# Optimization experiments

Measured on AMD Instinct MI355X. Metric: run time of the kernel, lower is better.

## Reference

```python
import jax, jax.numpy as jnp
import numpy as np

ROPE_BASE = 100.0  # CroCo/InfiniteVGGT-style 2D RoPE base

def _rope_1d(sub, pos, base=ROPE_BASE):
    # sub: (B,H,N,half), pos: (B,N) float
    half = sub.shape[-1]
    quarter = half // 2
    inv_freq = 1.0 / (base ** (jnp.arange(quarter, dtype=jnp.float32) / quarter))
    ang = pos[:, None, :, None] * inv_freq  # (B,1,N,quarter)
    cos, sin = jnp.cos(ang), jnp.sin(ang)
    x1, x2 = sub[..., :quarter], sub[..., quarter:]
    return jnp.concatenate([x1 * cos - x2 * sin, x1 * sin + x2 * cos], axis=-1)

def rope_2d(t, positions):
    # t: (B,H,N,Dh); positions: (B,N,2) int (y,x)
    Dh = t.shape[-1]
    half = Dh // 2
    pos_f = positions.astype(t.dtype)
    y = _rope_1d(t[..., :half], pos_f[..., 0])
    x = _rope_1d(t[..., half:], pos_f[..., 1])
    return jnp.concatenate([y, x], axis=-1)

def setup_inputs() -> dict:
    key = jax.random.key(0)
    k1, k2, k3, k4 = jax.random.split(key, 4)
    B, N, C, H = 2, 2048, 1024, 16
    x = jax.random.normal(k1, (B, N, C), dtype=jnp.float32)
    positions = jax.random.randint(k2, (B, N, 2), 0, 64, dtype=jnp.int32)
    qkv_w = jax.random.normal(k3, (3 * C, C), dtype=jnp.float32) * (C ** -0.5)
    proj_w = jax.random.normal(k4, (C, C), dtype=jnp.float32) * (C ** -0.5)
    proj_b = jnp.zeros((C,), dtype=jnp.float32)
    return {"x": x, "positions": positions, "qkv_w": qkv_w, "proj_w": proj_w, "proj_b": proj_b}

def reference(x, positions, qkv_w, proj_w, proj_b):
    B, N, C = x.shape
    H = 16
    Dh = C // H
    scale = Dh ** -0.5
    qkv = (x @ qkv_w.T).reshape(B, N, 3, H, Dh).transpose(2, 0, 3, 1, 4)  # (3,B,H,N,Dh)
    q, k, v = qkv[0], qkv[1], qkv[2]
    q = rope_2d(q, positions)
    k = rope_2d(k, positions)
    attn = jnp.einsum('bhnd,bhmd->bhnm', q, k) * scale  # (B,H,N,N)
    attn = jax.nn.softmax(attn, axis=-1)
    out = jnp.einsum('bhnm,bhmd->bhnd', attn, v)  # (B,H,N,Dh)
    out = out.transpose(0, 2, 1, 3).reshape(B, N, C)
    return out @ proj_w.T + proj_b
```

## Files before the change

kernel.cpp:

```cpp
#include <hip/hip_runtime.h>

typedef unsigned short u16;
typedef unsigned int   u32;
typedef __attribute__((ext_vector_type(8))) __bf16 bf16x8;
typedef __attribute__((ext_vector_type(4))) float  f32x4;

constexpr int BB = 2, SEQ = 2048, CH = 1024, NH = 16, DH = 64;

__device__ inline u16 f2bf(float f) {
    u32 u = __builtin_bit_cast(u32, f);
    u += 0x7FFF + ((u >> 16) & 1);
    return (u16)(u >> 16);
}
__device__ inline float bf2f(u16 b) { return __builtin_bit_cast(float, (u32)b << 16); }
__device__ inline u32 pkbf(float a, float b) {
    return (u32)f2bf(a) | ((u32)f2bf(b) << 16);
}
__device__ inline float fexp2(float x) {
#if __has_builtin(__builtin_amdgcn_exp2f)
    return __builtin_amdgcn_exp2f(x);
#else
    return exp2f(x);
#endif
}

__device__ inline void gld_lds16(const void* g, void* l) {
    __builtin_amdgcn_global_load_lds((const __attribute__((address_space(1))) void*)g,
                                     (__attribute__((address_space(3))) void*)l, 16, 0, 0);
}
__device__ inline f32x4 mfma16(bf16x8 a, bf16x8 b, f32x4 c) {
    return __builtin_amdgcn_mfma_f32_16x16x32_bf16(a, b, c, 0, 0, 0);
}
__device__ inline bf16x8 ld_frag(const u16* p) {
    return __builtin_bit_cast(bf16x8, *(const uint4*)p);
}

__global__ __launch_bounds__(256) void convert_kernel(const float* __restrict__ x,
                                                      const float* __restrict__ wq,
                                                      const float* __restrict__ wp,
                                                      u16* __restrict__ xb,
                                                      u16* __restrict__ wqb,
                                                      u16* __restrict__ wpb) {
    const int q = blockIdx.x * 256 + threadIdx.x;
    const float* src; u16* dst; int idx;
    if (q < 1048576)            { src = x;  dst = xb;  idx = q; }
    else if (q < 1048576+786432){ src = wq; dst = wqb; idx = q - 1048576; }
    else                        { src = wp; dst = wpb; idx = q - 1048576 - 786432; }
    float4 v = *(const float4*)(src + (size_t)idx * 4);
    ushort4 o; o.x = f2bf(v.x); o.y = f2bf(v.y); o.z = f2bf(v.z); o.w = f2bf(v.w);
    *(ushort4*)(dst + (size_t)idx * 4) = o;
}

__global__ __launch_bounds__(256) void gemm_bf16(const u16* __restrict__ A,
                                                 const u16* __restrict__ Bw,
                                                 const float* __restrict__ bias,
                                                 void* __restrict__ Cout,
                                                 int M, int N, int K, int out_fp32) {
    __shared__ u16 As[128 * 32];
    __shared__ u16 Bs[128 * 32];
    const int t = threadIdx.x, lane = t & 63, w = t >> 6;
    const int l15 = lane & 15, quad = lane >> 4;
    const int wm = w >> 1, wn = w & 1;
    const int m0 = blockIdx.y * 128, n0 = blockIdx.x * 128;

    const int row0 = t >> 2, v0 = t & 3;
    const int gi0 = (v0 - (row0 >> 1)) & 3;
    const int row1 = row0 + 64;
    const int gi1 = (v0 - (row1 >> 1)) & 3;

    f32x4 acc[4][4] = {};
    for (int k0 = 0; k0 < K; k0 += 32) {
        __syncthreads();
        gld_lds16(A  + (size_t)(m0 + row0) * K + k0 + gi0 * 8, As + t * 8);
        gld_lds16(A  + (size_t)(m0 + row1) * K + k0 + gi1 * 8, As + 2048 + t * 8);
        gld_lds16(Bw + (size_t)(n0 + row0) * K + k0 + gi0 * 8, Bs + t * 8);
        gld_lds16(Bw + (size_t)(n0 + row1) * K + k0 + gi1 * 8, Bs + 2048 + t * 8);
        __syncthreads();
        bf16x8 af[4], bfv[4];
#pragma unroll
        for (int mi = 0; mi < 4; ++mi) {
            const int r = wm * 64 + mi * 16 + l15;
            af[mi] = ld_frag(As + (r * 4 + ((quad + (r >> 1)) & 3)) * 8);
        }
#pragma unroll
        for (int nj = 0; nj < 4; ++nj) {
            const int r = wn * 64 + nj * 16 + l15;
            bfv[nj] = ld_frag(Bs + (r * 4 + ((quad + (r >> 1)) & 3)) * 8);
        }
#pragma unroll
        for (int mi = 0; mi < 4; ++mi)
#pragma unroll
            for (int nj = 0; nj < 4; ++nj)
                acc[mi][nj] = mfma16(af[mi], bfv[nj], acc[mi][nj]);
    }
    if (out_fp32) {
        float* C = (float*)Cout;
#pragma unroll
        for (int mi = 0; mi < 4; ++mi)
#pragma unroll
            for (int nj = 0; nj < 4; ++nj) {
                const int n = n0 + wn * 64 + nj * 16 + l15;
                const float bv = bias ? bias[n] : 0.0f;
#pragma unroll
                for (int r = 0; r < 4; ++r) {
                    const int m = m0 + wm * 64 + mi * 16 + quad * 4 + r;
                    C[(size_t)m * N + n] = acc[mi][nj][r] + bv;
                }
            }
    } else {
        u16* C = (u16*)Cout;
#pragma unroll
        for (int mi = 0; mi < 4; ++mi)
#pragma unroll
            for (int nj = 0; nj < 4; ++nj) {
                const int n = n0 + wn * 64 + nj * 16 + l15;
#pragma unroll
                for (int r = 0; r < 4; ++r) {
                    const int m = m0 + wm * 64 + mi * 16 + quad * 4 + r;
                    C[(size_t)m * N + n] = f2bf(acc[mi][nj][r]);
                }
            }
    }
}

__global__ __launch_bounds__(256) void rope_pack(const u16* __restrict__ qkv,
                                                 const int* __restrict__ pos,
                                                 u16* __restrict__ Qb,
                                                 u16* __restrict__ Kb,
                                                 u16* __restrict__ Vt) {
    __shared__ u16 vlds[64 * 68];
    const int t = threadIdx.x;
    const int r = t >> 2, s = t & 3;
    const int bh = blockIdx.y, b = bh >> 4;
    const int n0 = blockIdx.x * 64;
    const int bn = b * SEQ + n0 + r;
    const float py = (float)pos[bn * 2], px = (float)pos[bn * 2 + 1];

    float cy[4], sy[4], cx[4], sx[4];
#pragma unroll
    for (int j = 0; j < 4; ++j) {
        const int i = s * 4 + j;
        const float f = exp2f(-(float)i * 0.41524101186092f);
        sincosf(py * f, &sy[j], &cy[j]);
        sincosf(px * f, &sx[j], &cx[j]);
    }
    const size_t rowb = (size_t)bn * (3 * CH) + (bh & 15) * 64;

#pragma unroll
    for (int wk = 0; wk < 2; ++wk) {
        const u16* src = qkv + rowb + wk * CH;
        u16* dst = (wk ? Kb : Qb) + ((size_t)bh * SEQ + n0 + r) * 64;
        ushort4 a0 = *(const ushort4*)(src + s * 4);
        ushort4 a1 = *(const ushort4*)(src + s * 4 + 16);
        ushort4 a2 = *(const ushort4*)(src + s * 4 + 32);
        ushort4 a3 = *(const ushort4*)(src + s * 4 + 48);
        const float scale = wk ? 1.0f : 0.18033688011112042f;
        ushort4 o0, o1, o2, o3;
#pragma unroll
        for (int j = 0; j < 4; ++j) {
            const float x1 = bf2f(((const u16*)&a0)[j]), x2 = bf2f(((const u16*)&a1)[j]);
            ((u16*)&o0)[j] = f2bf((x1 * cy[j] - x2 * sy[j]) * scale);
            ((u16*)&o1)[j] = f2bf((x1 * sy[j] + x2 * cy[j]) * scale);
            const float y1 = bf2f(((const u16*)&a2)[j]), y2 = bf2f(((const u16*)&a3)[j]);
            ((u16*)&o2)[j] = f2bf((y1 * cx[j] - y2 * sx[j]) * scale);
            ((u16*)&o3)[j] = f2bf((y1 * sx[j] + y2 * cx[j]) * scale);
        }
        *(ushort4*)(dst + s * 4)      = o0;
        *(ushort4*)(dst + s * 4 + 16) = o1;
        *(ushort4*)(dst + s * 4 + 32) = o2;
        *(ushort4*)(dst + s * 4 + 48) = o3;
    }
    {
        const u16* src = qkv + rowb + 2 * CH;
#pragma unroll
        for (int jj = 0; jj < 4; ++jj) {
            ushort4 v = *(const ushort4*)(src + s * 16 + jj * 4);
#pragma unroll
            for (int j = 0; j < 4; ++j)
                vlds[(s * 16 + jj * 4 + j) * 68 + r] = ((const u16*)&v)[j];
        }
        __syncthreads();
        const int d = r;
        u16* gdst = Vt + ((size_t)bh * 64 + d) * SEQ + n0 + s * 16;
#pragma unroll
        for (int jj = 0; jj < 4; ++jj)
            *(ushort4*)(gdst + jj * 4) = *(const ushort4*)(vlds + d * 68 + s * 16 + jj * 4);
    }
}

__global__ __launch_bounds__(256, 4) void attn_mfma(const u16* __restrict__ Qb,
                                                    const u16* __restrict__ Kb,
                                                    const u16* __restrict__ Vt,
                                                    u16* __restrict__ Opart,
                                                    float* __restrict__ lpart) {
    __shared__ u16 Ks[64 * 64];
    __shared__ u16 Vs[64 * 64];
    __shared__ u16 Ps[128 * 72];
    const int t = threadIdx.x, lane = t & 63, w = t >> 6;
    const int l15 = lane & 15, quad = lane >> 4;
    const int bh = blockIdx.y;
    const int q0 = blockIdx.x * 128;
    const int z  = blockIdx.z;

    const int rowA = t >> 3, vA = t & 7;
    const int giA = (vA - rowA) & 7;
    const int rowB = rowA + 32;
    const int giB = (vA - rowB) & 7;

    const size_t kbase = (size_t)bh * SEQ * 64;
    const size_t vbase = (size_t)bh * 64 * SEQ;

    bf16x8 aq[2][2];
#pragma unroll
    for (int mi = 0; mi < 2; ++mi)
#pragma unroll
        for (int ks = 0; ks < 2; ++ks)
            aq[mi][ks] = ld_frag(Qb + ((size_t)bh * SEQ + q0 + w * 32 + mi * 16 + l15) * 64
                                 + ks * 32 + quad * 8);

    f32x4 oacc[2][4] = {};
    float lsum[2] = {0.0f, 0.0f};

    for (int kt = 0; kt < 16; ++kt) {
        const int k0 = z * 1024 + kt * 64;
        __syncthreads();
        gld_lds16(Kb + kbase + (size_t)(k0 + rowA) * 64 + giA * 8, Ks + t * 8);
        gld_lds16(Kb + kbase + (size_t)(k0 + rowB) * 64 + giB * 8, Ks + 2048 + t * 8);
        gld_lds16(Vt + vbase + (size_t)rowA * SEQ + k0 + giA * 8, Vs + t * 8);
        gld_lds16(Vt + vbase + (size_t)rowB * SEQ + k0 + giB * 8, Vs + 2048 + t * 8);
        __syncthreads();

        f32x4 sacc[2][4] = {};
#pragma unroll
        for (int ks = 0; ks < 2; ++ks)
#pragma unroll
            for (int nk = 0; nk < 4; ++nk) {
                const int rK = nk * 16 + l15;
                const bf16x8 kf = ld_frag(Ks + (rK * 8 + (((ks * 4 + quad) + rK) & 7)) * 8);
                sacc[0][nk] = mfma16(kf, aq[0][ks], sacc[0][nk]);
                sacc[1][nk] = mfma16(kf, aq[1][ks], sacc[1][nk]);
            }

#pragma unroll
        for (int mi = 0; mi < 2; ++mi) {
            const int prow = (w * 32 + mi * 16 + l15) * 72;
#pragma unroll
            for (int nk = 0; nk < 4; ++nk) {
                const float p0 = fexp2(sacc[mi][nk][0]);
                const float p1 = fexp2(sacc[mi][nk][1]);
                const float p2 = fexp2(sacc[mi][nk][2]);
                const float p3 = fexp2(sacc[mi][nk][3]);
                lsum[mi] += (p0 + p1) + (p2 + p3);
                uint2 pk; pk.x = pkbf(p0, p1); pk.y = pkbf(p2, p3);
                *(uint2*)&Ps[prow + nk * 16 + quad * 4] = pk;
            }
        }

#pragma unroll
        for (int ks = 0; ks < 2; ++ks) {
            const bf16x8 ap0 = ld_frag(Ps + (w * 32 + l15) * 72 + ks * 32 + quad * 8);
            const bf16x8 ap1 = ld_frag(Ps + (w * 32 + 16 + l15) * 72 + ks * 32 + quad * 8);
#pragma unroll
            for (int nj = 0; nj < 4; ++nj) {
                const int rV = nj * 16 + l15;
                const bf16x8 vf = ld_frag(Vs + (rV * 8 + (((ks * 4 + quad) + rV) & 7)) * 8);
                oacc[0][nj] = mfma16(ap0, vf, oacc[0][nj]);
                oacc[1][nj] = mfma16(ap1, vf, oacc[1][nj]);
            }
        }
    }

#pragma unroll
    for (int mi = 0; mi < 2; ++mi) {
        lsum[mi] += __shfl_xor(lsum[mi], 16);
        lsum[mi] += __shfl_xor(lsum[mi], 32);
        if (quad == 0)
            lpart[((size_t)z * 32 + bh) * SEQ + q0 + w * 32 + mi * 16 + l15] = lsum[mi];
#pragma unroll
        for (int r = 0; r < 4; ++r) {
            const int qrow = q0 + w * 32 + mi * 16 + quad * 4 + r;
            const size_t orow = (((size_t)z * 32 + bh) * SEQ + qrow) * 64;
#pragma unroll
            for (int nj = 0; nj < 4; ++nj)
                Opart[orow + nj * 16 + l15] = f2bf(oacc[mi][nj][r]);
        }
    }
}

__global__ __launch_bounds__(256) void merge_kernel(const u16* __restrict__ Opart,
                                                    const float* __restrict__ lpart,
                                                    u16* __restrict__ Ob) {
    const int gid = blockIdx.x * 256 + threadIdx.x;
    const int d4 = gid & 15, q = (gid >> 4) & 2047, bh = gid >> 15;
    const size_t i1 = ((size_t)bh * SEQ + q) * 64 + d4 * 4;
    const size_t i2 = i1 + (size_t)32 * SEQ * 64;
    const float inv = 1.0f / (lpart[(size_t)bh * SEQ + q] +
                              lpart[(size_t)(32 + bh) * SEQ + q]);
    const ushort4 a = *(const ushort4*)(Opart + i1);
    const ushort4 b = *(const ushort4*)(Opart + i2);
    ushort4 o;
    o.x = f2bf((bf2f(a.x) + bf2f(b.x)) * inv);
    o.y = f2bf((bf2f(a.y) + bf2f(b.y)) * inv);
    o.z = f2bf((bf2f(a.z) + bf2f(b.z)) * inv);
    o.w = f2bf((bf2f(a.w) + bf2f(b.w)) * inv);
    const int b_ = bh >> 4, h = bh & 15;
    *(ushort4*)(Ob + ((size_t)(b_ * SEQ + q)) * CH + h * 64 + d4 * 4) = o;
}

extern "C" void kernel_launch(void* const* d_in, const int* in_sizes, int n_in,
                              void* d_out, int out_size, void* d_ws, size_t ws_size,
                              hipStream_t stream) {
    const float* x      = (const float*)d_in[0];
    const int*   pos    = (const int*)d_in[1];
    const float* qkv_w  = (const float*)d_in[2];
    const float* proj_w = (const float*)d_in[3];
    const float* proj_b = (const float*)d_in[4];
    float* out = (float*)d_out;

    u16* ws = (u16*)d_ws;
    u16* qkv_bf  = ws;
    u16* Opart   = ws;
    u16* attn_bf = ws + 8388608;
    u16* x_bf    = ws + 12582912;
    u16* Qb      = x_bf;
    u16* wq_bf   = ws + 16777216;
    float* lpart = (float*)(ws + 16777216);
    u16* wp_bf   = ws + 19922944;
    u16* Kb      = ws + 20971520;
    u16* Vt      = ws + 25165824;

    const int M = BB * SEQ;

    convert_kernel<<<8192, 256, 0, stream>>>(x, qkv_w, proj_w, x_bf, wq_bf, wp_bf);
    gemm_bf16<<<dim3(3 * CH / 128, M / 128), 256, 0, stream>>>(
        x_bf, wq_bf, nullptr, qkv_bf, M, 3 * CH, CH, 0);
    rope_pack<<<dim3(SEQ / 64, BB * NH), 256, 0, stream>>>(qkv_bf, pos, Qb, Kb, Vt);
    attn_mfma<<<dim3(SEQ / 128, BB * NH, 2), 256, 0, stream>>>(Qb, Kb, Vt, Opart, lpart);
    merge_kernel<<<4096, 256, 0, stream>>>(Opart, lpart, attn_bf);
    gemm_bf16<<<dim3(CH / 128, M / 128), 256, 0, stream>>>(
        attn_bf, wp_bf, proj_b, out, M, CH, CH, 1);
}
```

Baseline: 215.0 us.

## Fuse RoPE and V transpose into QKV GEMM epilogue; MFMA row sums

Drops the separate rope_pack kernel. The QKV GEMM epilogue now applies RoPE and the Q scale directly to the accumulators and writes Q/K in head layout, and it transposes V through LDS before writing it out. This removes the round trip of the intermediate bf16 QKV tensor through memory and one kernel launch. In attention, the softmax row sums are now computed by an extra MFMA against a vector of ones on the bf16 P tile instead of scalar adds and shuffles, and pkbf uses the hardware packed bf16 convert when it is available. The costs are per-element sincos in the GEMM epilogue, scattered 2-byte stores for Q/K, and row sums taken from the rounded bf16 probabilities.

```diff
diff --git a/kernel.cpp b/kernel.cpp
--- a/kernel.cpp
+++ b/kernel.cpp
@@ -1,8 +1,10 @@
 #include <hip/hip_runtime.h>
+#include <cmath>
 
 typedef unsigned short u16;
 typedef unsigned int   u32;
 typedef __attribute__((ext_vector_type(8))) __bf16 bf16x8;
+typedef __attribute__((ext_vector_type(2))) __bf16 bf16x2;
 typedef __attribute__((ext_vector_type(4))) float  f32x4;
 
 constexpr int BB = 2, SEQ = 2048, CH = 1024, NH = 16, DH = 64;
@@ -14,7 +16,12 @@
 }
 __device__ inline float bf2f(u16 b) { return __builtin_bit_cast(float, (u32)b << 16); }
 __device__ inline u32 pkbf(float a, float b) {
+#if __has_builtin(__builtin_amdgcn_cvt_pk_bf16_f32)
+    bf16x2 r = __builtin_amdgcn_cvt_pk_bf16_f32(a, b);
+    return __builtin_bit_cast(u32, r);
+#else
     return (u32)f2bf(a) | ((u32)f2bf(b) << 16);
+#endif
 }
 __device__ inline float fexp2(float x) {
 #if __has_builtin(__builtin_amdgcn_exp2f)
@@ -51,11 +58,103 @@
     *(ushort4*)(dst + (size_t)idx * 4) = o;
 }
 
+__global__ __launch_bounds__(256) void gemm_qkv_rope(const u16* __restrict__ A,
+                                                     const u16* __restrict__ Bw,
+                                                     const int* __restrict__ pos,
+                                                     u16* __restrict__ Qb,
+                                                     u16* __restrict__ Kb,
+                                                     u16* __restrict__ Vt) {
+    __shared__ u16 smem[18432];
+    u16* As = smem;
+    u16* Bs = smem + 4096;
+    const int t = threadIdx.x, lane = t & 63, w = t >> 6;
+    const int l15 = lane & 15, quad = lane >> 4;
+    const int wm = w >> 1, wn = w & 1;
+    const int m0 = blockIdx.y * 128, n0 = blockIdx.x * 128;
+    const int K = CH, N = 3 * CH;
+
+    const int row0 = t >> 2, v0 = t & 3;
+    const int gi0 = (v0 - (row0 >> 1)) & 3;
+    const int row1 = row0 + 64;
+    const int gi1 = (v0 - (row1 >> 1)) & 3;
+
+    f32x4 acc[4][4] = {};
+    for (int k0 = 0; k0 < K; k0 += 32) {
+        __syncthreads();
+        gld_lds16(A  + (size_t)(m0 + row0) * K + k0 + gi0 * 8, As + t * 8);
+        gld_lds16(A  + (size_t)(m0 + row1) * K + k0 + gi1 * 8, As + 2048 + t * 8);
+        gld_lds16(Bw + (size_t)(n0 + row0) * K + k0 + gi0 * 8, Bs + t * 8);
+        gld_lds16(Bw + (size_t)(n0 + row1) * K + k0 + gi1 * 8, Bs + 2048 + t * 8);
+        __syncthreads();
+        bf16x8 af[4], bfv[4];
+#pragma unroll
+        for (int mi = 0; mi < 4; ++mi) {
+            const int r = wm * 64 + mi * 16 + l15;
+            af[mi] = ld_frag(As + (r * 4 + ((quad + (r >> 1)) & 3)) * 8);
+        }
+#pragma unroll
+        for (int nj = 0; nj < 4; ++nj) {
+            const int r = wn * 64 + nj * 16 + l15;
+            bfv[nj] = ld_frag(Bs + (r * 4 + ((quad + (r >> 1)) & 3)) * 8);
+        }
+#pragma unroll
+        for (int mi = 0; mi < 4; ++mi)
+#pragma unroll
+            for (int nj = 0; nj < 4; ++nj)
+                acc[mi][nj] = mfma16(af[mi], bfv[nj], acc[mi][nj]);
+    }
+
+    const int reg = n0 >> 10;
+    const int h   = ((n0 & 1023) >> 6) + wn;
+    if (reg < 2) {
+        const float fr = exp2f(-(float)l15 * 0.41524101186092f);
+        const float scale = reg ? 1.0f : 0.18033688011112042f;
+        u16* dst = reg ? Kb : Qb;
+#pragma unroll
+        for (int mi = 0; mi < 4; ++mi) {
+#pragma unroll
+            for (int r = 0; r < 4; ++r) {
+                const int m = m0 + wm * 64 + mi * 16 + quad * 4 + r;
+                const int bh = (m >> 11) * NH + h;
+                const int n  = m & 2047;
+                float sy, cy, sx, cx;
+                sincosf((float)pos[m * 2]     * fr, &sy, &cy);
+                sincosf((float)pos[m * 2 + 1] * fr, &sx, &cx);
+                cy *= scale; sy *= scale; cx *= scale; sx *= scale;
+                const float x1 = acc[mi][0][r], x2 = acc[mi][1][r];
+                const float y1 = acc[mi][2][r], y2 = acc[mi][3][r];
+                u16* p = dst + ((size_t)bh * SEQ + n) * 64 + l15;
+                p[0]  = f2bf(x1 * cy - x2 * sy);
+                p[16] = f2bf(x1 * sy + x2 * cy);
+                p[32] = f2bf(y1 * cx - y2 * sx);
+                p[48] = f2bf(y1 * sx + y2 * cx);
+            }
+        }
+    } else {
+        __syncthreads();
+        u16* T = smem + w * 4608;
+#pragma unroll
+        for (int mi = 0; mi < 4; ++mi)
+#pragma unroll
+            for (int nj = 0; nj < 4; ++nj)
+#pragma unroll
+                for (int r = 0; r < 4; ++r)
+                    T[(nj * 16 + l15) * 72 + mi * 16 + quad * 4 + r] =
+                        f2bf(acc[mi][nj][r]);
+        const int bh = (m0 >> 11) * NH + h;
+        const int nbase = (m0 & 2047) + wm * 64;
+        u16* gdst = Vt + ((size_t)bh * 64 + lane) * SEQ + nbase;
+#pragma unroll
+        for (int j = 0; j < 8; ++j)
+            *(uint4*)(gdst + j * 8) = *(const uint4*)(T + lane * 72 + j * 8);
+    }
+}
+
 __global__ __launch_bounds__(256) void gemm_bf16(const u16* __restrict__ A,
                                                  const u16* __restrict__ Bw,
                                                  const float* __restrict__ bias,
-                                                 void* __restrict__ Cout,
-                                                 int M, int N, int K, int out_fp32) {
+                                                 float* __restrict__ C,
+                                                 int M, int N, int K) {
     __shared__ u16 As[128 * 32];
     __shared__ u16 Bs[128 * 32];
     const int t = threadIdx.x, lane = t & 63, w = t >> 6;
@@ -93,99 +192,18 @@
             for (int nj = 0; nj < 4; ++nj)
                 acc[mi][nj] = mfma16(af[mi], bfv[nj], acc[mi][nj]);
     }
-    if (out_fp32) {
-        float* C = (float*)Cout;
-#pragma unroll
-        for (int mi = 0; mi < 4; ++mi)
-#pragma unroll
-            for (int nj = 0; nj < 4; ++nj) {
-                const int n = n0 + wn * 64 + nj * 16 + l15;
-                const float bv = bias ? bias[n] : 0.0f;
-#pragma unroll
-                for (int r = 0; r < 4; ++r) {
-                    const int m = m0 + wm * 64 + mi * 16 + quad * 4 + r;
-                    C[(size_t)m * N + n] = acc[mi][nj][r] + bv;
-                }
-            }
-    } else {
-        u16* C = (u16*)Cout;
-#pragma unroll
-        for (int mi = 0; mi < 4; ++mi)
-#pragma unroll
-            for (int nj = 0; nj < 4; ++nj) {
-                const int n = n0 + wn * 64 + nj * 16 + l15;
-#pragma unroll
-                for (int r = 0; r < 4; ++r) {
-                    const int m = m0 + wm * 64 + mi * 16 + quad * 4 + r;
-                    C[(size_t)m * N + n] = f2bf(acc[mi][nj][r]);
-                }
-            }
-    }
-}
-
-__global__ __launch_bounds__(256) void rope_pack(const u16* __restrict__ qkv,
-                                                 const int* __restrict__ pos,
-                                                 u16* __restrict__ Qb,
-                                                 u16* __restrict__ Kb,
-                                                 u16* __restrict__ Vt) {
-    __shared__ u16 vlds[64 * 68];
-    const int t = threadIdx.x;
-    const int r = t >> 2, s = t & 3;
-    const int bh = blockIdx.y, b = bh >> 4;
-    const int n0 = blockIdx.x * 64;
-    const int bn = b * SEQ + n0 + r;
-    const float py = (float)pos[bn * 2], px = (float)pos[bn * 2 + 1];
-
-    float cy[4], sy[4], cx[4], sx[4];
-#pragma unroll
-    for (int j = 0; j < 4; ++j) {
-        const int i = s * 4 + j;
-        const float f = exp2f(-(float)i * 0.41524101186092f);
-        sincosf(py * f, &sy[j], &cy[j]);
-        sincosf(px * f, &sx[j], &cx[j]);
-    }
-    const size_t rowb = (size_t)bn * (3 * CH) + (bh & 15) * 64;
-
-#pragma unroll
-    for (int wk = 0; wk < 2; ++wk) {
-        const u16* src = qkv + rowb + wk * CH;
-        u16* dst = (wk ? Kb : Qb) + ((size_t)bh * SEQ + n0 + r) * 64;
-        ushort4 a0 = *(const ushort4*)(src + s * 4);
-        ushort4 a1 = *(const ushort4*)(src + s * 4 + 16);
-        ushort4 a2 = *(const ushort4*)(src + s * 4 + 32);
-        ushort4 a3 = *(const ushort4*)(src + s * 4 + 48);
-        const float scale = wk ? 1.0f : 0.18033688011112042f;
-        ushort4 o0, o1, o2, o3;
-#pragma unroll
-        for (int j = 0; j < 4; ++j) {
-            const float x1 = bf2f(((const u16*)&a0)[j]), x2 = bf2f(((const u16*)&a1)[j]);
-            ((u16*)&o0)[j] = f2bf((x1 * cy[j] - x2 * sy[j]) * scale);
-            ((u16*)&o1)[j] = f2bf((x1 * sy[j] + x2 * cy[j]) * scale);
-            const float y1 = bf2f(((const u16*)&a2)[j]), y2 = bf2f(((const u16*)&a3)[j]);
-            ((u16*)&o2)[j] = f2bf((y1 * cx[j] - y2 * sx[j]) * scale);
-            ((u16*)&o3)[j] = f2bf((y1 * sx[j] + y2 * cx[j]) * scale);
-        }
-        *(ushort4*)(dst + s * 4)      = o0;
-        *(ushort4*)(dst + s * 4 + 16) = o1;
-        *(ushort4*)(dst + s * 4 + 32) = o2;
-        *(ushort4*)(dst + s * 4 + 48) = o3;
-    }
-    {
-        const u16* src = qkv + rowb + 2 * CH;
-#pragma unroll
-        for (int jj = 0; jj < 4; ++jj) {
-            ushort4 v = *(const ushort4*)(src + s * 16 + jj * 4);
-#pragma unroll
-            for (int j = 0; j < 4; ++j)
-                vlds[(s * 16 + jj * 4 + j) * 68 + r] = ((const u16*)&v)[j];
-        }
-        __syncthreads();
-        const int d = r;
-        u16* gdst = Vt + ((size_t)bh * 64 + d) * SEQ + n0 + s * 16;
-#pragma unroll
-        for (int jj = 0; jj < 4; ++jj)
-            *(ushort4*)(gdst + jj * 4) = *(const ushort4*)(vlds + d * 68 + s * 16 + jj * 4);
-    }
+#pragma unroll
+    for (int mi = 0; mi < 4; ++mi)
+#pragma unroll
+        for (int nj = 0; nj < 4; ++nj) {
+            const int n = n0 + wn * 64 + nj * 16 + l15;
+            const float bv = bias[n];
+#pragma unroll
+            for (int r = 0; r < 4; ++r) {
+                const int m = m0 + wm * 64 + mi * 16 + quad * 4 + r;
+                C[(size_t)m * N + n] = acc[mi][nj][r] + bv;
+            }
+        }
 }
 
 __global__ __launch_bounds__(256, 4) void attn_mfma(const u16* __restrict__ Qb,
@@ -210,6 +228,9 @@
     const size_t kbase = (size_t)bh * SEQ * 64;
     const size_t vbase = (size_t)bh * 64 * SEQ;
 
+    const uint4 ones_u = {0x3F803F80u, 0x3F803F80u, 0x3F803F80u, 0x3F803F80u};
+    const bf16x8 onesf = __builtin_bit_cast(bf16x8, ones_u);
+
     bf16x8 aq[2][2];
 #pragma unroll
     for (int mi = 0; mi < 2; ++mi)
@@ -219,7 +240,7 @@
                                  + ks * 32 + quad * 8);
 
     f32x4 oacc[2][4] = {};
-    float lsum[2] = {0.0f, 0.0f};
+    f32x4 lacc[2] = {};
 
     for (int kt = 0; kt < 16; ++kt) {
         const int k0 = z * 1024 + kt * 64;
@@ -250,7 +271,6 @@
                 const float p1 = fexp2(sacc[mi][nk][1]);
                 const float p2 = fexp2(sacc[mi][nk][2]);
                 const float p3 = fexp2(sacc[mi][nk][3]);
-                lsum[mi] += (p0 + p1) + (p2 + p3);
                 uint2 pk; pk.x = pkbf(p0, p1); pk.y = pkbf(p2, p3);
                 *(uint2*)&Ps[prow + nk * 16 + quad * 4] = pk;
             }
@@ -260,6 +280,8 @@
         for (int ks = 0; ks < 2; ++ks) {
             const bf16x8 ap0 = ld_frag(Ps + (w * 32 + l15) * 72 + ks * 32 + quad * 8);
             const bf16x8 ap1 = ld_frag(Ps + (w * 32 + 16 + l15) * 72 + ks * 32 + quad * 8);
+            lacc[0] = mfma16(ap0, onesf, lacc[0]);
+            lacc[1] = mfma16(ap1, onesf, lacc[1]);
 #pragma unroll
             for (int nj = 0; nj < 4; ++nj) {
                 const int rV = nj * 16 + l15;
@@ -271,20 +293,17 @@
     }
 
 #pragma unroll
-    for (int mi = 0; mi < 2; ++mi) {
-        lsum[mi] += __shfl_xor(lsum[mi], 16);
-        lsum[mi] += __shfl_xor(lsum[mi], 32);
-        if (quad == 0)
-            lpart[((size_t)z * 32 + bh) * SEQ + q0 + w * 32 + mi * 16 + l15] = lsum[mi];
+    for (int mi = 0; mi < 2; ++mi)
 #pragma unroll
         for (int r = 0; r < 4; ++r) {
             const int qrow = q0 + w * 32 + mi * 16 + quad * 4 + r;
+            if (l15 == 0)
+                lpart[((size_t)z * 32 + bh) * SEQ + qrow] = lacc[mi][r];
             const size_t orow = (((size_t)z * 32 + bh) * SEQ + qrow) * 64;
 #pragma unroll
             for (int nj = 0; nj < 4; ++nj)
                 Opart[orow + nj * 16 + l15] = f2bf(oacc[mi][nj][r]);
         }
-    }
 }
 
 __global__ __launch_bounds__(256) void merge_kernel(const u16* __restrict__ Opart,
@@ -318,25 +337,23 @@
     float* out = (float*)d_out;
 
     u16* ws = (u16*)d_ws;
-    u16* qkv_bf  = ws;
-    u16* Opart   = ws;
-    u16* attn_bf = ws + 8388608;
-    u16* x_bf    = ws + 12582912;
-    u16* Qb      = x_bf;
-    u16* wq_bf   = ws + 16777216;
-    float* lpart = (float*)(ws + 16777216);
-    u16* wp_bf   = ws + 19922944;
-    u16* Kb      = ws + 20971520;
-    u16* Vt      = ws + 25165824;
+    u16* x_bf    = ws;
+    u16* attn_bf = ws;
+    u16* wq_bf   = ws + 4194304;
+    float* lpart = (float*)(ws + 4194304);
+    u16* wp_bf   = ws + 7340032;
+    u16* Qb      = ws + 8388608;
+    u16* Kb      = ws + 12582912;
+    u16* Vt      = ws + 16777216;
+    u16* Opart   = ws + 20971520;
 
     const int M = BB * SEQ;
 
     convert_kernel<<<8192, 256, 0, stream>>>(x, qkv_w, proj_w, x_bf, wq_bf, wp_bf);
-    gemm_bf16<<<dim3(3 * CH / 128, M / 128), 256, 0, stream>>>(
-        x_bf, wq_bf, nullptr, qkv_bf, M, 3 * CH, CH, 0);
-    rope_pack<<<dim3(SEQ / 64, BB * NH), 256, 0, stream>>>(qkv_bf, pos, Qb, Kb, Vt);
+    gemm_qkv_rope<<<dim3(3 * CH / 128, M / 128), 256, 0, stream>>>(
+        x_bf, wq_bf, pos, Qb, Kb, Vt);
     attn_mfma<<<dim3(SEQ / 128, BB * NH, 2), 256, 0, stream>>>(Qb, Kb, Vt, Opart, lpart);
     merge_kernel<<<4096, 256, 0, stream>>>(Opart, lpart, attn_bf);
     gemm_bf16<<<dim3(CH / 128, M / 128), 256, 0, stream>>>(
-        attn_bf, wp_bf, proj_b, out, M, CH, CH, 1);
-}
+        attn_bf, wp_bf, proj_b, out, M, CH, CH);
+}
```

After: 218.3 us. No clear change (+1.5%).
